# Performance work log

Hardware: AMD Instinct MI355X
Metric: run time of the kernel (lower is better)

The kernel has to match this reference:

```python
import jax, jax.numpy as jnp
import numpy as np

H = 16          # attention_head_num
DH = 64         # attention_head_size
D = H * DH      # out_dim / model dim
SIZE_PER_HEAD = 64  # scaling denominator (init arg, used as sqrt divisor)


def setup_inputs() -> dict:
    key = jax.random.key(0)
    ks = jax.random.split(key, 12)
    B, S = 2, 2048
    scale = 1.0 / np.sqrt(D)
    inp = {
        "qx": jax.random.normal(ks[0], (B, S, D), dtype=jnp.float32),
        "kx": jax.random.normal(ks[1], (B, S, D), dtype=jnp.float32),
        "vx": jax.random.normal(ks[2], (B, S, D), dtype=jnp.float32),
        "Wq": jax.random.normal(ks[3], (D, D), dtype=jnp.float32) * scale,
        "bq": jnp.zeros((D,), dtype=jnp.float32),
        "Wk": jax.random.normal(ks[4], (D, D), dtype=jnp.float32) * scale,
        "bk": jnp.zeros((D,), dtype=jnp.float32),
        "Wv": jax.random.normal(ks[5], (D, D), dtype=jnp.float32) * scale,
        "bv": jnp.zeros((D,), dtype=jnp.float32),
        "Wo": jax.random.normal(ks[6], (D, D), dtype=jnp.float32) * scale,
        "bo": jnp.zeros((D,), dtype=jnp.float32),
    }
    return inp


def reference(qx, kx, vx, Wq, bq, Wk, bk, Wv, bv, Wo, bo):
    B, Sq, _ = qx.shape
    Sk = kx.shape[1]
    # QKV projections
    q = qx @ Wq + bq  # [B,Sq,D]
    k = kx @ Wk + bk  # [B,Sk,D]
    v = vx @ Wv + bv  # [B,Sk,D]
    # split heads -> [B,H,S,DH]
    q = q.reshape(B, Sq, H, DH).transpose(0, 2, 1, 3)
    k = k.reshape(B, Sk, H, DH).transpose(0, 2, 1, 3)
    v = v.reshape(B, Sk, H, DH).transpose(0, 2, 1, 3)
    # scores [B,H,Sq,Sk]; NOTE: original divides by sqrt(size_per_head)
    scores = jnp.einsum("bhqd,bhkd->bhqk", q, k) / jnp.sqrt(
        jnp.asarray(SIZE_PER_HEAD, dtype=q.dtype)
    )
    probs = jax.nn.softmax(scores, axis=-1)
    ctx = jnp.einsum("bhqk,bhkd->bhqd", probs, v)  # [B,H,Sq,DH]
    ctx = ctx.transpose(0, 2, 1, 3).reshape(B, Sq, D)
    return ctx @ Wo + bo
```

## Files before the change

kernel.cpp:

```cpp
#include <hip/hip_runtime.h>

typedef _Float16 half_t;
typedef _Float16 half8 __attribute__((ext_vector_type(8)));
typedef __fp16 fp16x2 __attribute__((ext_vector_type(2)));
typedef float f32x16 __attribute__((ext_vector_type(16)));
typedef float f32x4v __attribute__((ext_vector_type(4)));
typedef unsigned uint2v __attribute__((ext_vector_type(2)));

#define MFMA32(A, B, C) __builtin_amdgcn_mfma_f32_32x32x16_f16(A, B, C, 0, 0, 0)

#if __has_builtin(__builtin_amdgcn_exp2f)
#define EXP2F(x) __builtin_amdgcn_exp2f(x)
#else
#define EXP2F(x) exp2f(x)
#endif

static constexpr int S = 2048;
static constexpr int D = 1024;
static constexpr float QSCALE = 0.18033688011112042f;


__device__ __forceinline__ void gload_lds16(const void* g, void* l) {
    __builtin_amdgcn_global_load_lds(
        (const __attribute__((address_space(1))) unsigned int*)g,
        (__attribute__((address_space(3))) unsigned int*)l, 16, 0, 0);
}

__global__ __launch_bounds__(256) void cvtw(
    const float* __restrict__ x0, const float* __restrict__ x1, const float* __restrict__ x2,
    const float* __restrict__ w0, const float* __restrict__ w1,
    const float* __restrict__ w2, const float* __restrict__ w3,
    half_t* __restrict__ o0, half_t* __restrict__ o1, half_t* __restrict__ o2,
    half_t* __restrict__ wt)
{
    __shared__ char sm[33280];
    int y = blockIdx.y;
    int t = threadIdx.x;
    if (y < 3) {
        float (*tile)[65] = (float(*)[65])sm;
        const float* src = (y == 0) ? x0 : (y == 1) ? x1 : x2;
        half_t* dst = (y == 0) ? o0 : (y == 1) ? o1 : o2;
        int mt = blockIdx.x >> 4, kt = blockIdx.x & 15;
        const float* sbase = src + (size_t)(mt * 128) * D + kt * 64;
        int rr = t >> 4, col = (t & 15) * 4;
#pragma unroll
        for (int p = 0; p < 8; ++p) {
            int row = rr + p * 16;
            f32x4v v = *(const f32x4v*)(sbase + (size_t)row * D + col);
            tile[row][col] = v[0]; tile[row][col + 1] = v[1];
            tile[row][col + 2] = v[2]; tile[row][col + 3] = v[3];
        }
        __syncthreads();
        int c = t >> 5, r0 = t & 31;
        half_t* dbase = dst + ((size_t)(mt * 16 + kt)) * 8192;
#pragma unroll
        for (int i = 0; i < 4; ++i) {
            int row = r0 + 32 * i;
            half8 h;
#pragma unroll
            for (int j = 0; j < 8; ++j) h[j] = (half_t)tile[row][c * 8 + j];
            *(half8*)(dbase + ((size_t)c * 128 + row) * 8) = h;
        }
    } else {
        float (*tile)[129] = (float(*)[129])sm;
        int w = blockIdx.x >> 7;
        const float* W = (w == 0) ? w0 : (w == 1) ? w1 : (w == 2) ? w2 : w3;
        int idx = blockIdx.x & 127;
        int nt = idx >> 4, kt = idx & 15;
        const float* sbase = W + (size_t)(kt * 64) * D + nt * 128;
        int kr = t >> 5, col = (t & 31) * 4;
#pragma unroll
        for (int p = 0; p < 8; ++p) {
            int k = kr + p * 8;
            f32x4v v = *(const f32x4v*)(sbase + (size_t)k * D + col);
            tile[k][col] = v[0]; tile[k][col + 1] = v[1];
            tile[k][col + 2] = v[2]; tile[k][col + 3] = v[3];
        }
        __syncthreads();
        int c = t >> 5, r0 = t & 31;
        half_t* dbase = wt + (size_t)w * 1048576 + ((size_t)(nt * 16 + kt)) * 8192;
#pragma unroll
        for (int i = 0; i < 4; ++i) {
            int n = r0 + 32 * i;
            half8 h;
#pragma unroll
            for (int j = 0; j < 8; ++j) h[j] = (half_t)tile[c * 8 + j][n];
            *(half8*)(dbase + ((size_t)c * 128 + n) * 8) = h;
        }
    }
}

__global__ __launch_bounds__(256, 4) void gemm_qkv(
    const half_t* __restrict__ a0, const half_t* __restrict__ a1, const half_t* __restrict__ a2,
    const half_t* __restrict__ wt,
    const float* __restrict__ b0, const float* __restrict__ b1, const float* __restrict__ b2,
    half_t* __restrict__ qh, half_t* __restrict__ kh, half_t* __restrict__ vt)
{
    __shared__ char smem[32768];
    half_t* As = (half_t*)smem;
    half_t* Bs = (half_t*)(smem + 16384);
    int z = blockIdx.z;
    const half_t* A = (z == 0) ? a0 : (z == 1) ? a1 : a2;
    const half_t* BT = wt + (size_t)z * 1048576;
    const float* bias = (z == 0) ? b0 : (z == 1) ? b1 : b2;
    int L = blockIdx.x;
    int w = L >> 3;
    int mt = (L & 7) * 4 + (w & 3);
    int nt8 = w >> 2;
    int m0 = mt * 128, n0 = nt8 * 128;
    int tid = threadIdx.x, lane = tid & 63, wave = tid >> 6;
    int ml = lane & 31, hi = lane >> 5;
    int wm = (wave & 1) * 64, wn = (wave >> 1) * 64;

    f32x16 acc00 = {}, acc01 = {}, acc10 = {}, acc11 = {};

    for (int kt = 0; kt < 16; ++kt) {
        __syncthreads();
        const half_t* Aslab = A + ((size_t)(mt * 16 + kt)) * 8192;
        const half_t* Bslab = BT + ((size_t)(nt8 * 16 + kt)) * 8192;
#pragma unroll
        for (int j = 0; j < 4; ++j) {
            int s = wave * 4 + j;
            gload_lds16(Aslab + s * 512 + lane * 8, As + s * 512);
            gload_lds16(Bslab + s * 512 + lane * 8, Bs + s * 512);
        }
        __syncthreads();
#pragma unroll
        for (int ks = 0; ks < 4; ++ks) {
            int co = (2 * ks + hi) * 128;
            half8 af0 = *(const half8*)(As + (size_t)(co + wm + ml) * 8);
            half8 af1 = *(const half8*)(As + (size_t)(co + wm + 32 + ml) * 8);
            half8 bf0 = *(const half8*)(Bs + (size_t)(co + wn + ml) * 8);
            half8 bf1 = *(const half8*)(Bs + (size_t)(co + wn + 32 + ml) * 8);
            acc00 = MFMA32(af0, bf0, acc00);
            acc01 = MFMA32(af0, bf1, acc01);
            acc10 = MFMA32(af1, bf0, acc10);
            acc11 = MFMA32(af1, bf1, acc11);
        }
    }

    __syncthreads();
    half_t* buf = (half_t*)smem;
#pragma unroll
    for (int nt = 0; nt < 2; ++nt) {
        int nl = wn + nt * 32 + ml;
        float bv = bias[n0 + nl];
        int hh = nl >> 6, c = (nl >> 3) & 7, j = nl & 7, dd = nl & 63;
#pragma unroll
        for (int mt2 = 0; mt2 < 2; ++mt2) {
            f32x16 av = (mt2 == 0) ? (nt == 0 ? acc00 : acc01) : (nt == 0 ? acc10 : acc11);
#pragma unroll
            for (int r = 0; r < 16; ++r) {
                int rl = wm + mt2 * 32 + 4 * hi + (r & 3) + 8 * (r >> 2);
                float v = av[r] + bv;
                if (z == 0) v *= QSCALE;
                if (z <= 1) {
                    buf[((rl * 2 + hh) * 8 + (c ^ (rl & 7))) * 8 + j] = (half_t)v;
                } else {
                    int cc = rl >> 3, js = rl & 7;
                    buf[((dd * 2 + hh) * 16 + (cc ^ (dd & 7))) * 8 + js] = (half_t)v;
                }
            }
        }
    }
    __syncthreads();
    int bq_ = m0 >> 11, skt = (m0 >> 7) & 15, h0 = n0 >> 6;
    half_t* dstm = (z == 0) ? qh : (z == 1) ? kh : vt;
#pragma unroll
    for (int i = 0; i < 8; ++i) {
        int o = tid + 256 * i;
        int hh = o >> 10;
        half_t* gdst = dstm + ((size_t)(bq_ * 16 + h0 + hh)) * 131072 + (size_t)skt * 8192;
        half8 v8;
        int off;
        if (z <= 1) {
            int c = (o >> 7) & 7, r = o & 127;
            v8 = *(const half8*)(buf + (((r * 2 + hh) * 8 + (c ^ (r & 7))) * 8));
            off = (c * 128 + r) * 8;
        } else {
            int cc = (o >> 6) & 15, dd = o & 63;
            v8 = *(const half8*)(buf + (((dd * 2 + hh) * 16 + (cc ^ (dd & 7))) * 8));
            off = (cc * 64 + dd) * 8;
        }
        *(half8*)(gdst + off) = v8;
    }
}

__global__ __launch_bounds__(256, 4) void gemm_out(
    const half_t* __restrict__ A, const half_t* __restrict__ BT,
    const float* __restrict__ bias, float* __restrict__ out)
{
    __shared__ char smem[32768];
    half_t* As = (half_t*)smem;
    half_t* Bs = (half_t*)(smem + 16384);
    int L = blockIdx.x;
    int w = L >> 3;
    int mt = (L & 7) * 4 + (w & 3);
    int nt8 = w >> 2;
    int m0 = mt * 128, n0 = nt8 * 128;
    int tid = threadIdx.x, lane = tid & 63, wave = tid >> 6;
    int ml = lane & 31, hi = lane >> 5;
    int wm = (wave & 1) * 64, wn = (wave >> 1) * 64;

    f32x16 acc00 = {}, acc01 = {}, acc10 = {}, acc11 = {};

    for (int kt = 0; kt < 16; ++kt) {
        __syncthreads();
        const half_t* Aslab = A + ((size_t)(mt * 16 + kt)) * 8192;
        const half_t* Bslab = BT + ((size_t)(nt8 * 16 + kt)) * 8192;
#pragma unroll
        for (int j = 0; j < 4; ++j) {
            int s = wave * 4 + j;
            gload_lds16(Aslab + s * 512 + lane * 8, As + s * 512);
            gload_lds16(Bslab + s * 512 + lane * 8, Bs + s * 512);
        }
        __syncthreads();
#pragma unroll
        for (int ks = 0; ks < 4; ++ks) {
            int co = (2 * ks + hi) * 128;
            half8 af0 = *(const half8*)(As + (size_t)(co + wm + ml) * 8);
            half8 af1 = *(const half8*)(As + (size_t)(co + wm + 32 + ml) * 8);
            half8 bf0 = *(const half8*)(Bs + (size_t)(co + wn + ml) * 8);
            half8 bf1 = *(const half8*)(Bs + (size_t)(co + wn + 32 + ml) * 8);
            acc00 = MFMA32(af0, bf0, acc00);
            acc01 = MFMA32(af0, bf1, acc01);
            acc10 = MFMA32(af1, bf0, acc10);
            acc11 = MFMA32(af1, bf1, acc11);
        }
    }

#pragma unroll
    for (int nt = 0; nt < 2; ++nt) {
        int n = n0 + wn + nt * 32 + ml;
        float bv = bias[n];
#pragma unroll
        for (int mt2 = 0; mt2 < 2; ++mt2) {
            f32x16 av = (mt2 == 0) ? (nt == 0 ? acc00 : acc01) : (nt == 0 ? acc10 : acc11);
            int rbase = m0 + wm + mt2 * 32 + 4 * hi;
#pragma unroll
            for (int r = 0; r < 16; ++r) {
                int row = rbase + (r & 3) + 8 * (r >> 2);
                out[(size_t)row * D + n] = av[r] + bv;
            }
        }
    }
}

__global__ __launch_bounds__(512, 4) void attn(
    const half_t* __restrict__ qh, const half_t* __restrict__ kh,
    const half_t* __restrict__ vt, half_t* __restrict__ ctx)
{
    __shared__ char smem[65536];

    int L = blockIdx.x;
    int slot = L >> 3;
    int bh = (L & 7) + 8 * (slot >> 4);
    int sq = slot & 15;
    int b_ = bh >> 4, h = bh & 15;

    int tid = threadIdx.x, lane = tid & 63, wave = tid >> 6;
    int ml = lane & 31, hi = lane >> 5;
    int qq = wave & 3, th = wave >> 2;
    const half_t* qslab = qh + (size_t)bh * 131072 + (size_t)sq * 8192;
    const half_t* khead = kh + (size_t)bh * 131072;
    const half_t* vhead = vt + (size_t)bh * 131072;

    {
        half_t* QB = (half_t*)(smem + 32768);
        half_t* K0 = (half_t*)(smem);
        half_t* V0 = (half_t*)(smem + 16384);
#pragma unroll
        for (int j = 0; j < 2; ++j) {
            int s = wave * 2 + j;
            gload_lds16(qslab + s * 512 + lane * 8, QB + s * 512);
            gload_lds16(khead + s * 512 + lane * 8, K0 + s * 512);
            gload_lds16(vhead + s * 512 + lane * 8, V0 + s * 512);
        }
    }
    __syncthreads();
    half8 qf[4];
    {
        half_t* QB = (half_t*)(smem + 32768);
#pragma unroll
        for (int ks = 0; ks < 4; ++ks)
            qf[ks] = *(const half8*)(QB + ((size_t)((2 * ks + hi) * 128 + qq * 32 + ml)) * 8);
    }
    __syncthreads();

    f32x16 oacc[2] = {};
    float lsumA = 0.0f, lsumB = 0.0f;
    fp16x2 one2; one2.x = (__fp16)1.0f; one2.y = (__fp16)1.0f;
    const f32x16 sinit = {-10.0f, -10.0f, -10.0f, -10.0f, -10.0f, -10.0f, -10.0f, -10.0f,
                          -10.0f, -10.0f, -10.0f, -10.0f, -10.0f, -10.0f, -10.0f, -10.0f};

    int t0 = th * 2, t1 = th * 2 + 1;

    for (int it = 0; it < 16; ++it) {
        int bb = it & 1;
        if (it < 15) {
            const half_t* kslab = khead + (size_t)(it + 1) * 8192;
            const half_t* vslab = vhead + (size_t)(it + 1) * 8192;
            half_t* Kd = (half_t*)(smem + (bb ^ 1) * 32768);
            half_t* Vd = (half_t*)(smem + 16384 + (bb ^ 1) * 32768);
#pragma unroll
            for (int j = 0; j < 2; ++j) {
                int s = wave * 2 + j;
                gload_lds16(kslab + s * 512 + lane * 8, Kd + s * 512);
                gload_lds16(vslab + s * 512 + lane * 8, Vd + s * 512);
            }
        }
        half_t* Ks  = (half_t*)(smem + bb * 32768);
        half_t* VTs = (half_t*)(smem + 16384 + bb * 32768);

        f32x16 sv0 = sinit, sv1 = sinit;
        __builtin_amdgcn_s_setprio(1);
#pragma unroll
        for (int ks = 0; ks < 4; ++ks) {
            half8 kf0 = *(const half8*)(Ks + ((size_t)((2 * ks + hi) * 128 + t0 * 32 + ml)) * 8);
            half8 kf1 = *(const half8*)(Ks + ((size_t)((2 * ks + hi) * 128 + t1 * 32 + ml)) * 8);
            sv0 = MFMA32(kf0, qf[ks], sv0);
            sv1 = MFMA32(kf1, qf[ks], sv1);
        }
        __builtin_amdgcn_s_setprio(0);

        unsigned pkv0[8];
        {
            float lsA = lsumA;
#pragma unroll
            for (int j = 0; j < 8; ++j) {
                float pa = EXP2F(sv0[2 * j]);
                float pb = EXP2F(sv0[2 * j + 1]);
#if __has_builtin(__builtin_amdgcn_cvt_pkrtz)
                fp16x2 h2 = __builtin_amdgcn_cvt_pkrtz(pa, pb);
#else
                fp16x2 h2; h2.x = (__fp16)pa; h2.y = (__fp16)pb;
#endif
                pkv0[j] = __builtin_bit_cast(unsigned, h2);
#if __has_builtin(__builtin_amdgcn_fdot2)
                lsA = __builtin_amdgcn_fdot2(h2, one2, lsA, false);
#else
                lsA += pa + pb;
#endif
            }
            lsumA = lsA;
        }

#pragma unroll
        for (int kp = 0; kp < 2; ++kp) {
            union { unsigned u[4]; half8 h; } fr;
#if __has_builtin(__builtin_amdgcn_permlane32_swap)
            uint2v w0 = __builtin_amdgcn_permlane32_swap(pkv0[4 * kp + 0], pkv0[4 * kp + 2], false, false);
            uint2v w1 = __builtin_amdgcn_permlane32_swap(pkv0[4 * kp + 1], pkv0[4 * kp + 3], false, false);
            fr.u[0] = w0.x; fr.u[1] = w1.x; fr.u[2] = w0.y; fr.u[3] = w1.y;
#else
            unsigned e0 = pkv0[4 * kp + 0], e1 = pkv0[4 * kp + 1];
            unsigned o0 = pkv0[4 * kp + 2], o1 = pkv0[4 * kp + 3];
            unsigned s0u = hi ? e0 : o0, s1u = hi ? e1 : o1;
            unsigned k0u = hi ? o0 : e0, k1u = hi ? o1 : e1;
            unsigned r0 = __shfl_xor(s0u, 32, 64);
            unsigned r1 = __shfl_xor(s1u, 32, 64);
            fr.u[0] = hi ? r0 : k0u; fr.u[1] = hi ? r1 : k1u;
            fr.u[2] = hi ? k0u : r0; fr.u[3] = hi ? k1u : r1;
#endif
            __builtin_amdgcn_s_setprio(1);
#pragma unroll
            for (int dt = 0; dt < 2; ++dt) {
                half8 vf = *(const half8*)(VTs + ((size_t)((4 * t0 + 2 * kp + hi) * 64 + dt * 32 + ml)) * 8);
                oacc[dt] = MFMA32(fr.h, vf, oacc[dt]);
            }
            __builtin_amdgcn_s_setprio(0);
        }

        unsigned pkv1[8];
        {
            float lsB = lsumB;
#pragma unroll
            for (int j = 0; j < 8; ++j) {
                float pa = EXP2F(sv1[2 * j]);
                float pb = EXP2F(sv1[2 * j + 1]);
#if __has_builtin(__builtin_amdgcn_cvt_pkrtz)
                fp16x2 h2 = __builtin_amdgcn_cvt_pkrtz(pa, pb);
#else
                fp16x2 h2; h2.x = (__fp16)pa; h2.y = (__fp16)pb;
#endif
                pkv1[j] = __builtin_bit_cast(unsigned, h2);
#if __has_builtin(__builtin_amdgcn_fdot2)
                lsB = __builtin_amdgcn_fdot2(h2, one2, lsB, false);
#else
                lsB += pa + pb;
#endif
            }
            lsumB = lsB;
        }

#pragma unroll
        for (int kp = 0; kp < 2; ++kp) {
            union { unsigned u[4]; half8 h; } fr;
#if __has_builtin(__builtin_amdgcn_permlane32_swap)
            uint2v w0 = __builtin_amdgcn_permlane32_swap(pkv1[4 * kp + 0], pkv1[4 * kp + 2], false, false);
            uint2v w1 = __builtin_amdgcn_permlane32_swap(pkv1[4 * kp + 1], pkv1[4 * kp + 3], false, false);
            fr.u[0] = w0.x; fr.u[1] = w1.x; fr.u[2] = w0.y; fr.u[3] = w1.y;
#else
            unsigned e0 = pkv1[4 * kp + 0], e1 = pkv1[4 * kp + 1];
            unsigned o0 = pkv1[4 * kp + 2], o1 = pkv1[4 * kp + 3];
            unsigned s0u = hi ? e0 : o0, s1u = hi ? e1 : o1;
            unsigned k0u = hi ? o0 : e0, k1u = hi ? o1 : e1;
            unsigned r0 = __shfl_xor(s0u, 32, 64);
            unsigned r1 = __shfl_xor(s1u, 32, 64);
            fr.u[0] = hi ? r0 : k0u; fr.u[1] = hi ? r1 : k1u;
            fr.u[2] = hi ? k0u : r0; fr.u[3] = hi ? k1u : r1;
#endif
            __builtin_amdgcn_s_setprio(1);
#pragma unroll
            for (int dt = 0; dt < 2; ++dt) {
                half8 vf = *(const half8*)(VTs + ((size_t)((4 * t1 + 2 * kp + hi) * 64 + dt * 32 + ml)) * 8);
                oacc[dt] = MFMA32(fr.h, vf, oacc[dt]);
            }
            __builtin_amdgcn_s_setprio(0);
        }

        __syncthreads();
    }

    float lsum = lsumA + lsumB;
    float lt = lsum + __shfl_xor(lsum, 32, 64);

    float* OB = (float*)(smem + (size_t)qq * 8192);
    if (th == 1) {
#pragma unroll
        for (int dt = 0; dt < 2; ++dt)
#pragma unroll
            for (int r = 0; r < 16; ++r) {
                int q = 4 * hi + (r & 3) + 8 * (r >> 2);
                OB[q * 64 + dt * 32 + ml] = oacc[dt][r];
            }
    }
    __syncthreads();
    if (th == 0) {
#pragma unroll
        for (int dt = 0; dt < 2; ++dt)
#pragma unroll
            for (int r = 0; r < 16; ++r) {
                int q = 4 * hi + (r & 3) + 8 * (r >> 2);
                oacc[dt][r] += OB[q * 64 + dt * 32 + ml];
            }
    }
    __syncthreads();
    float* Lbuf = (float*)(smem + 32768);
    if (th == 1 && hi == 0) Lbuf[qq * 32 + ml] = lt;
    __syncthreads();
    if (th == 0 && hi == 0) Lbuf[qq * 32 + ml] += lt;
    __syncthreads();
    if (th == 0) {
        half_t* cslab = ctx + ((size_t)((b_ * 16 + sq) * 16 + h)) * 8192;
#pragma unroll
        for (int dt = 0; dt < 2; ++dt)
#pragma unroll
            for (int r = 0; r < 16; ++r) {
                int qw = 4 * hi + (r & 3) + 8 * (r >> 2);
                int q = qq * 32 + qw;
                int d = dt * 32 + ml;
                float linv = __builtin_amdgcn_rcpf(Lbuf[q]);
                cslab[((d >> 3) * 128 + q) * 8 + (d & 7)] =
                    (half_t)(oacc[dt][r] * linv);
            }
    }
}

extern "C" void kernel_launch(void* const* d_in, const int* in_sizes, int n_in,
                              void* d_out, int out_size, void* d_ws, size_t ws_size,
                              hipStream_t stream)
{
    const float* qx = (const float*)d_in[0];
    const float* kx = (const float*)d_in[1];
    const float* vx = (const float*)d_in[2];
    const float* Wq = (const float*)d_in[3];
    const float* bq = (const float*)d_in[4];
    const float* Wk = (const float*)d_in[5];
    const float* bk = (const float*)d_in[6];
    const float* Wv = (const float*)d_in[7];
    const float* bv = (const float*)d_in[8];
    const float* Wo = (const float*)d_in[9];
    const float* bo = (const float*)d_in[10];
    float* out = (float*)d_out;

    half_t* ws = (half_t*)d_ws;
    const size_t NT = (size_t)4096 * 1024;
    half_t* qxh = ws;
    half_t* kxh = qxh + NT;
    half_t* vxh = kxh + NT;
    half_t* wt = vxh + NT;
    half_t* qh = wt + (size_t)4 * 1048576;
    half_t* kh = qh + NT;
    half_t* vtr = kh + NT;
    half_t* ctx = vtr + NT;

    cvtw<<<dim3(512, 4), 256, 0, stream>>>(qx, kx, vx, Wq, Wk, Wv, Wo, qxh, kxh, vxh, wt);
    gemm_qkv<<<dim3(256, 1, 3), 256, 0, stream>>>(qxh, kxh, vxh, wt, bq, bk, bv, qh, kh, vtr);
    attn<<<dim3(512, 1, 1), 512, 0, stream>>>(qh, kh, vtr, ctx);
    gemm_out<<<dim3(256, 1, 1), 256, 0, stream>>>(ctx, wt + (size_t)3 * 1048576, bo, out);
}
```

Before: 215.2 us.

## Fuse all four stages into one persistent kernel with grid barriers

Measured after the change: 610.7 us. +183.8%, slower.

```diff
diff --git a/kernel.cpp b/kernel.cpp
--- a/kernel.cpp
+++ b/kernel.cpp
@@ -26,89 +26,43 @@
         (__attribute__((address_space(3))) unsigned int*)l, 16, 0, 0);
 }
 
-__global__ __launch_bounds__(256) void cvtw(
-    const float* __restrict__ x0, const float* __restrict__ x1, const float* __restrict__ x2,
-    const float* __restrict__ w0, const float* __restrict__ w1,
-    const float* __restrict__ w2, const float* __restrict__ w3,
-    half_t* __restrict__ o0, half_t* __restrict__ o1, half_t* __restrict__ o2,
-    half_t* __restrict__ wt)
-{
-    __shared__ char sm[33280];
-    int y = blockIdx.y;
-    int t = threadIdx.x;
-    if (y < 3) {
-        float (*tile)[65] = (float(*)[65])sm;
-        const float* src = (y == 0) ? x0 : (y == 1) ? x1 : x2;
-        half_t* dst = (y == 0) ? o0 : (y == 1) ? o1 : o2;
-        int mt = blockIdx.x >> 4, kt = blockIdx.x & 15;
-        const float* sbase = src + (size_t)(mt * 128) * D + kt * 64;
-        int rr = t >> 4, col = (t & 15) * 4;
-#pragma unroll
-        for (int p = 0; p < 8; ++p) {
-            int row = rr + p * 16;
-            f32x4v v = *(const f32x4v*)(sbase + (size_t)row * D + col);
-            tile[row][col] = v[0]; tile[row][col + 1] = v[1];
-            tile[row][col + 2] = v[2]; tile[row][col + 3] = v[3];
-        }
-        __syncthreads();
-        int c = t >> 5, r0 = t & 31;
-        half_t* dbase = dst + ((size_t)(mt * 16 + kt)) * 8192;
-#pragma unroll
-        for (int i = 0; i < 4; ++i) {
-            int row = r0 + 32 * i;
-            half8 h;
-#pragma unroll
-            for (int j = 0; j < 8; ++j) h[j] = (half_t)tile[row][c * 8 + j];
-            *(half8*)(dbase + ((size_t)c * 128 + row) * 8) = h;
-        }
-    } else {
-        float (*tile)[129] = (float(*)[129])sm;
-        int w = blockIdx.x >> 7;
-        const float* W = (w == 0) ? w0 : (w == 1) ? w1 : (w == 2) ? w2 : w3;
-        int idx = blockIdx.x & 127;
-        int nt = idx >> 4, kt = idx & 15;
-        const float* sbase = W + (size_t)(kt * 64) * D + nt * 128;
-        int kr = t >> 5, col = (t & 31) * 4;
-#pragma unroll
-        for (int p = 0; p < 8; ++p) {
-            int k = kr + p * 8;
-            f32x4v v = *(const f32x4v*)(sbase + (size_t)k * D + col);
-            tile[k][col] = v[0]; tile[k][col + 1] = v[1];
-            tile[k][col + 2] = v[2]; tile[k][col + 3] = v[3];
-        }
-        __syncthreads();
-        int c = t >> 5, r0 = t & 31;
-        half_t* dbase = wt + (size_t)w * 1048576 + ((size_t)(nt * 16 + kt)) * 8192;
-#pragma unroll
-        for (int i = 0; i < 4; ++i) {
-            int n = r0 + 32 * i;
-            half8 h;
-#pragma unroll
-            for (int j = 0; j < 8; ++j) h[j] = (half_t)tile[c * 8 + j][n];
-            *(half8*)(dbase + ((size_t)c * 128 + n) * 8) = h;
-        }
-    }
+__device__ __forceinline__ void gridbar(unsigned* bar, int idx) {
+    __syncthreads();
+    if (threadIdx.x == 0) {
+        __threadfence();
+        unsigned* cnt  = bar + idx * 16;
+        unsigned* flag = bar + idx * 16 + 8;
+        unsigned old = atomicAdd(cnt, 1u);
+        if (old == 511u) {
+            __hip_atomic_store(flag, 1u, __ATOMIC_RELEASE, __HIP_MEMORY_SCOPE_AGENT);
+        } else {
+            while (__hip_atomic_load(flag, __ATOMIC_ACQUIRE, __HIP_MEMORY_SCOPE_AGENT) == 0u)
+                __builtin_amdgcn_s_sleep(2);
+        }
+    }
+    __syncthreads();
+    __threadfence();
 }
 
-__global__ __launch_bounds__(256, 4) void gemm_qkv(
+__device__ __forceinline__ void gemm_tile_qkv(
+    int job, int t, char* sm, bool active,
     const half_t* __restrict__ a0, const half_t* __restrict__ a1, const half_t* __restrict__ a2,
     const half_t* __restrict__ wt,
     const float* __restrict__ b0, const float* __restrict__ b1, const float* __restrict__ b2,
-    half_t* __restrict__ qh, half_t* __restrict__ kh, half_t* __restrict__ vt)
+    half_t* __restrict__ qh, half_t* __restrict__ kh, half_t* __restrict__ vtb)
 {
-    __shared__ char smem[32768];
-    half_t* As = (half_t*)smem;
-    half_t* Bs = (half_t*)(smem + 16384);
-    int z = blockIdx.z;
+    half_t* As = (half_t*)sm;
+    half_t* Bs = (half_t*)(sm + 16384);
+    int z = job >> 8;
+    int L = job & 255;
     const half_t* A = (z == 0) ? a0 : (z == 1) ? a1 : a2;
     const half_t* BT = wt + (size_t)z * 1048576;
     const float* bias = (z == 0) ? b0 : (z == 1) ? b1 : b2;
-    int L = blockIdx.x;
     int w = L >> 3;
     int mt = (L & 7) * 4 + (w & 3);
     int nt8 = w >> 2;
     int m0 = mt * 128, n0 = nt8 * 128;
-    int tid = threadIdx.x, lane = tid & 63, wave = tid >> 6;
+    int lane = t & 63, wave = t >> 6;
     int ml = lane & 31, hi = lane >> 5;
     int wm = (wave & 1) * 64, wn = (wave >> 1) * 64;
 
@@ -116,89 +70,96 @@
 
     for (int kt = 0; kt < 16; ++kt) {
         __syncthreads();
-        const half_t* Aslab = A + ((size_t)(mt * 16 + kt)) * 8192;
-        const half_t* Bslab = BT + ((size_t)(nt8 * 16 + kt)) * 8192;
-#pragma unroll
-        for (int j = 0; j < 4; ++j) {
-            int s = wave * 4 + j;
-            gload_lds16(Aslab + s * 512 + lane * 8, As + s * 512);
-            gload_lds16(Bslab + s * 512 + lane * 8, Bs + s * 512);
-        }
-        __syncthreads();
-#pragma unroll
-        for (int ks = 0; ks < 4; ++ks) {
-            int co = (2 * ks + hi) * 128;
-            half8 af0 = *(const half8*)(As + (size_t)(co + wm + ml) * 8);
-            half8 af1 = *(const half8*)(As + (size_t)(co + wm + 32 + ml) * 8);
-            half8 bf0 = *(const half8*)(Bs + (size_t)(co + wn + ml) * 8);
-            half8 bf1 = *(const half8*)(Bs + (size_t)(co + wn + 32 + ml) * 8);
-            acc00 = MFMA32(af0, bf0, acc00);
-            acc01 = MFMA32(af0, bf1, acc01);
-            acc10 = MFMA32(af1, bf0, acc10);
-            acc11 = MFMA32(af1, bf1, acc11);
+        if (active) {
+            const half_t* Aslab = A + ((size_t)(mt * 16 + kt)) * 8192;
+            const half_t* Bslab = BT + ((size_t)(nt8 * 16 + kt)) * 8192;
+#pragma unroll
+            for (int j = 0; j < 4; ++j) {
+                int s = wave * 4 + j;
+                gload_lds16(Aslab + s * 512 + lane * 8, As + s * 512);
+                gload_lds16(Bslab + s * 512 + lane * 8, Bs + s * 512);
+            }
+        }
+        __syncthreads();
+        if (active) {
+#pragma unroll
+            for (int ks = 0; ks < 4; ++ks) {
+                int co = (2 * ks + hi) * 128;
+                half8 af0 = *(const half8*)(As + (size_t)(co + wm + ml) * 8);
+                half8 af1 = *(const half8*)(As + (size_t)(co + wm + 32 + ml) * 8);
+                half8 bf0 = *(const half8*)(Bs + (size_t)(co + wn + ml) * 8);
+                half8 bf1 = *(const half8*)(Bs + (size_t)(co + wn + 32 + ml) * 8);
+                acc00 = MFMA32(af0, bf0, acc00);
+                acc01 = MFMA32(af0, bf1, acc01);
+                acc10 = MFMA32(af1, bf0, acc10);
+                acc11 = MFMA32(af1, bf1, acc11);
+            }
         }
     }
 
     __syncthreads();
-    half_t* buf = (half_t*)smem;
-#pragma unroll
-    for (int nt = 0; nt < 2; ++nt) {
-        int nl = wn + nt * 32 + ml;
-        float bv = bias[n0 + nl];
-        int hh = nl >> 6, c = (nl >> 3) & 7, j = nl & 7, dd = nl & 63;
-#pragma unroll
-        for (int mt2 = 0; mt2 < 2; ++mt2) {
-            f32x16 av = (mt2 == 0) ? (nt == 0 ? acc00 : acc01) : (nt == 0 ? acc10 : acc11);
-#pragma unroll
-            for (int r = 0; r < 16; ++r) {
-                int rl = wm + mt2 * 32 + 4 * hi + (r & 3) + 8 * (r >> 2);
-                float v = av[r] + bv;
-                if (z == 0) v *= QSCALE;
-                if (z <= 1) {
-                    buf[((rl * 2 + hh) * 8 + (c ^ (rl & 7))) * 8 + j] = (half_t)v;
-                } else {
-                    int cc = rl >> 3, js = rl & 7;
-                    buf[((dd * 2 + hh) * 16 + (cc ^ (dd & 7))) * 8 + js] = (half_t)v;
+    half_t* buf = (half_t*)sm;
+    if (active) {
+#pragma unroll
+        for (int nt = 0; nt < 2; ++nt) {
+            int nl = wn + nt * 32 + ml;
+            float bv = bias[n0 + nl];
+            int hh = nl >> 6, c = (nl >> 3) & 7, j = nl & 7, dd = nl & 63;
+#pragma unroll
+            for (int mt2 = 0; mt2 < 2; ++mt2) {
+                f32x16 av = (mt2 == 0) ? (nt == 0 ? acc00 : acc01) : (nt == 0 ? acc10 : acc11);
+#pragma unroll
+                for (int r = 0; r < 16; ++r) {
+                    int rl = wm + mt2 * 32 + 4 * hi + (r & 3) + 8 * (r >> 2);
+                    float v = av[r] + bv;
+                    if (z == 0) v *= QSCALE;
+                    if (z <= 1) {
+                        buf[((rl * 2 + hh) * 8 + (c ^ (rl & 7))) * 8 + j] = (half_t)v;
+                    } else {
+                        int cc = rl >> 3, js = rl & 7;
+                        buf[((dd * 2 + hh) * 16 + (cc ^ (dd & 7))) * 8 + js] = (half_t)v;
+                    }
                 }
             }
         }
     }
     __syncthreads();
-    int bq_ = m0 >> 11, skt = (m0 >> 7) & 15, h0 = n0 >> 6;
-    half_t* dstm = (z == 0) ? qh : (z == 1) ? kh : vt;
-#pragma unroll
-    for (int i = 0; i < 8; ++i) {
-        int o = tid + 256 * i;
-        int hh = o >> 10;
-        half_t* gdst = dstm + ((size_t)(bq_ * 16 + h0 + hh)) * 131072 + (size_t)skt * 8192;
-        half8 v8;
-        int off;
-        if (z <= 1) {
-            int c = (o >> 7) & 7, r = o & 127;
-            v8 = *(const half8*)(buf + (((r * 2 + hh) * 8 + (c ^ (r & 7))) * 8));
-            off = (c * 128 + r) * 8;
-        } else {
-            int cc = (o >> 6) & 15, dd = o & 63;
-            v8 = *(const half8*)(buf + (((dd * 2 + hh) * 16 + (cc ^ (dd & 7))) * 8));
-            off = (cc * 64 + dd) * 8;
-        }
-        *(half8*)(gdst + off) = v8;
+    if (active) {
+        int bq_ = m0 >> 11, skt = (m0 >> 7) & 15, h0 = n0 >> 6;
+        half_t* dstm = (z == 0) ? qh : (z == 1) ? kh : vtb;
+#pragma unroll
+        for (int i = 0; i < 8; ++i) {
+            int o = t + 256 * i;
+            int hh = o >> 10;
+            half_t* gdst = dstm + ((size_t)(bq_ * 16 + h0 + hh)) * 131072 + (size_t)skt * 8192;
+            half8 v8;
+            int off;
+            if (z <= 1) {
+                int c = (o >> 7) & 7, r = o & 127;
+                v8 = *(const half8*)(buf + (((r * 2 + hh) * 8 + (c ^ (r & 7))) * 8));
+                off = (c * 128 + r) * 8;
+            } else {
+                int cc = (o >> 6) & 15, dd = o & 63;
+                v8 = *(const half8*)(buf + (((dd * 2 + hh) * 16 + (cc ^ (dd & 7))) * 8));
+                off = (cc * 64 + dd) * 8;
+            }
+            *(half8*)(gdst + off) = v8;
+        }
     }
 }
 
-__global__ __launch_bounds__(256, 4) void gemm_out(
+__device__ __forceinline__ void gemm_tile_out(
+    int L, int t, char* sm, bool active,
     const half_t* __restrict__ A, const half_t* __restrict__ BT,
     const float* __restrict__ bias, float* __restrict__ out)
 {
-    __shared__ char smem[32768];
-    half_t* As = (half_t*)smem;
-    half_t* Bs = (half_t*)(smem + 16384);
-    int L = blockIdx.x;
+    half_t* As = (half_t*)sm;
+    half_t* Bs = (half_t*)(sm + 16384);
     int w = L >> 3;
     int mt = (L & 7) * 4 + (w & 3);
     int nt8 = w >> 2;
     int m0 = mt * 128, n0 = nt8 * 128;
-    int tid = threadIdx.x, lane = tid & 63, wave = tid >> 6;
+    int lane = t & 63, wave = t >> 6;
     int ml = lane & 31, hi = lane >> 5;
     int wm = (wave & 1) * 64, wn = (wave >> 1) * 64;
 
@@ -206,264 +167,356 @@
 
     for (int kt = 0; kt < 16; ++kt) {
         __syncthreads();
-        const half_t* Aslab = A + ((size_t)(mt * 16 + kt)) * 8192;
-        const half_t* Bslab = BT + ((size_t)(nt8 * 16 + kt)) * 8192;
-#pragma unroll
-        for (int j = 0; j < 4; ++j) {
-            int s = wave * 4 + j;
-            gload_lds16(Aslab + s * 512 + lane * 8, As + s * 512);
-            gload_lds16(Bslab + s * 512 + lane * 8, Bs + s * 512);
-        }
-        __syncthreads();
-#pragma unroll
-        for (int ks = 0; ks < 4; ++ks) {
-            int co = (2 * ks + hi) * 128;
-            half8 af0 = *(const half8*)(As + (size_t)(co + wm + ml) * 8);
-            half8 af1 = *(const half8*)(As + (size_t)(co + wm + 32 + ml) * 8);
-            half8 bf0 = *(const half8*)(Bs + (size_t)(co + wn + ml) * 8);
-            half8 bf1 = *(const half8*)(Bs + (size_t)(co + wn + 32 + ml) * 8);
-            acc00 = MFMA32(af0, bf0, acc00);
-            acc01 = MFMA32(af0, bf1, acc01);
-            acc10 = MFMA32(af1, bf0, acc10);
-            acc11 = MFMA32(af1, bf1, acc11);
-        }
-    }
-
-#pragma unroll
-    for (int nt = 0; nt < 2; ++nt) {
-        int n = n0 + wn + nt * 32 + ml;
-        float bv = bias[n];
-#pragma unroll
-        for (int mt2 = 0; mt2 < 2; ++mt2) {
-            f32x16 av = (mt2 == 0) ? (nt == 0 ? acc00 : acc01) : (nt == 0 ? acc10 : acc11);
-            int rbase = m0 + wm + mt2 * 32 + 4 * hi;
-#pragma unroll
-            for (int r = 0; r < 16; ++r) {
-                int row = rbase + (r & 3) + 8 * (r >> 2);
-                out[(size_t)row * D + n] = av[r] + bv;
+        if (active) {
+            const half_t* Aslab = A + ((size_t)(mt * 16 + kt)) * 8192;
+            const half_t* Bslab = BT + ((size_t)(nt8 * 16 + kt)) * 8192;
+#pragma unroll
+            for (int j = 0; j < 4; ++j) {
+                int s = wave * 4 + j;
+                gload_lds16(Aslab + s * 512 + lane * 8, As + s * 512);
+                gload_lds16(Bslab + s * 512 + lane * 8, Bs + s * 512);
+            }
+        }
+        __syncthreads();
+        if (active) {
+#pragma unroll
+            for (int ks = 0; ks < 4; ++ks) {
+                int co = (2 * ks + hi) * 128;
+                half8 af0 = *(const half8*)(As + (size_t)(co + wm + ml) * 8);
+                half8 af1 = *(const half8*)(As + (size_t)(co + wm + 32 + ml) * 8);
+                half8 bf0 = *(const half8*)(Bs + (size_t)(co + wn + ml) * 8);
+                half8 bf1 = *(const half8*)(Bs + (size_t)(co + wn + 32 + ml) * 8);
+                acc00 = MFMA32(af0, bf0, acc00);
+                acc01 = MFMA32(af0, bf1, acc01);
+                acc10 = MFMA32(af1, bf0, acc10);
+                acc11 = MFMA32(af1, bf1, acc11);
+            }
+        }
+    }
+
+    if (active) {
+#pragma unroll
+        for (int nt = 0; nt < 2; ++nt) {
+            int n = n0 + wn + nt * 32 + ml;
+            float bv = bias[n];
+#pragma unroll
+            for (int mt2 = 0; mt2 < 2; ++mt2) {
+                f32x16 av = (mt2 == 0) ? (nt == 0 ? acc00 : acc01) : (nt == 0 ? acc10 : acc11);
+                int rbase = m0 + wm + mt2 * 32 + 4 * hi;
+#pragma unroll
+                for (int r = 0; r < 16; ++r) {
+                    int row = rbase + (r & 3) + 8 * (r >> 2);
+                    out[(size_t)row * D + n] = av[r] + bv;
+                }
             }
         }
     }
 }
 
-__global__ __launch_bounds__(512, 4) void attn(
-    const half_t* __restrict__ qh, const half_t* __restrict__ kh,
-    const half_t* __restrict__ vt, half_t* __restrict__ ctx)
+__global__ __launch_bounds__(512, 4) void fused(
+    const float* __restrict__ qx, const float* __restrict__ kx, const float* __restrict__ vx,
+    const float* __restrict__ Wq, const float* __restrict__ bq,
+    const float* __restrict__ Wk, const float* __restrict__ bk,
+    const float* __restrict__ Wv, const float* __restrict__ bv,
+    const float* __restrict__ Wo, const float* __restrict__ bo,
+    float* __restrict__ out,
+    half_t* __restrict__ qxh, half_t* __restrict__ kxh, half_t* __restrict__ vxh,
+    half_t* __restrict__ wt, half_t* __restrict__ qh, half_t* __restrict__ kh,
+    half_t* __restrict__ vtr, half_t* __restrict__ ctx, unsigned* __restrict__ bar)
 {
     __shared__ char smem[65536];
-
-    int L = blockIdx.x;
-    int slot = L >> 3;
-    int bh = (L & 7) + 8 * (slot >> 4);
-    int sq = slot & 15;
-    int b_ = bh >> 4, h = bh & 15;
-
-    int tid = threadIdx.x, lane = tid & 63, wave = tid >> 6;
-    int ml = lane & 31, hi = lane >> 5;
-    int qq = wave & 3, th = wave >> 2;
-    const half_t* qslab = qh + (size_t)bh * 131072 + (size_t)sq * 8192;
-    const half_t* khead = kh + (size_t)bh * 131072;
-    const half_t* vhead = vt + (size_t)bh * 131072;
+    int bid = blockIdx.x;
+    int t = threadIdx.x;
+    int sb = t >> 8, t256 = t & 255;
+
+    for (int job = bid; job < 2048; job += 512) {
+        __syncthreads();
+        int y = job >> 9, x = job & 511;
+        if (y < 3) {
+            float (*tile)[65] = (float(*)[65])smem;
+            const float* src = (y == 0) ? qx : (y == 1) ? kx : vx;
+            half_t* dst = (y == 0) ? qxh : (y == 1) ? kxh : vxh;
+            int mt = x >> 4, kt = x & 15;
+            const float* sbase = src + (size_t)(mt * 128) * D + kt * 64;
+            int rr = t >> 4, col = (t & 15) * 4;
+#pragma unroll
+            for (int p = 0; p < 4; ++p) {
+                int row = rr + p * 32;
+                f32x4v v = *(const f32x4v*)(sbase + (size_t)row * D + col);
+                tile[row][col] = v[0]; tile[row][col + 1] = v[1];
+                tile[row][col + 2] = v[2]; tile[row][col + 3] = v[3];
+            }
+            __syncthreads();
+            int c = t >> 6, r0 = t & 63;
+            half_t* dbase = dst + ((size_t)(mt * 16 + kt)) * 8192;
+#pragma unroll
+            for (int i = 0; i < 2; ++i) {
+                int row = r0 + 64 * i;
+                half8 h;
+#pragma unroll
+                for (int j = 0; j < 8; ++j) h[j] = (half_t)tile[row][c * 8 + j];
+                *(half8*)(dbase + ((size_t)c * 128 + row) * 8) = h;
+            }
+        } else {
+            float (*tile)[129] = (float(*)[129])smem;
+            int w = x >> 7;
+            const float* W = (w == 0) ? Wq : (w == 1) ? Wk : (w == 2) ? Wv : Wo;
+            int idx = x & 127;
+            int nt = idx >> 4, kt = idx & 15;
+            const float* sbase = W + (size_t)(kt * 64) * D + nt * 128;
+            int kr = t >> 5, col = (t & 31) * 4;
+#pragma unroll
+            for (int p = 0; p < 4; ++p) {
+                int k = kr + p * 16;
+                f32x4v v = *(const f32x4v*)(sbase + (size_t)k * D + col);
+                tile[k][col] = v[0]; tile[k][col + 1] = v[1];
+                tile[k][col + 2] = v[2]; tile[k][col + 3] = v[3];
+            }
+            __syncthreads();
+            int c = t >> 6, r0 = t & 63;
+            half_t* dbase = wt + (size_t)w * 1048576 + ((size_t)(nt * 16 + kt)) * 8192;
+#pragma unroll
+            for (int i = 0; i < 2; ++i) {
+                int n = r0 + 64 * i;
+                half8 h;
+#pragma unroll
+                for (int j = 0; j < 8; ++j) h[j] = (half_t)tile[c * 8 + j][n];
+                *(half8*)(dbase + ((size_t)c * 128 + n) * 8) = h;
+            }
+        }
+    }
+    gridbar(bar, 0);
 
     {
-        half_t* QB = (half_t*)(smem + 32768);
-        half_t* K0 = (half_t*)(smem);
-        half_t* V0 = (half_t*)(smem + 16384);
-#pragma unroll
-        for (int j = 0; j < 2; ++j) {
-            int s = wave * 2 + j;
-            gload_lds16(qslab + s * 512 + lane * 8, QB + s * 512);
-            gload_lds16(khead + s * 512 + lane * 8, K0 + s * 512);
-            gload_lds16(vhead + s * 512 + lane * 8, V0 + s * 512);
-        }
-    }
-    __syncthreads();
-    half8 qf[4];
+        int job; bool active;
+        if (sb == 0) { job = bid; active = true; }
+        else { job = 512 + (bid >> 1); active = ((bid & 1) == 0); }
+        gemm_tile_qkv(active ? job : 0, t256, smem + (size_t)sb * 32768, active,
+                      qxh, kxh, vxh, wt, bq, bk, bv, qh, kh, vtr);
+    }
+    gridbar(bar, 1);
+
     {
-        half_t* QB = (half_t*)(smem + 32768);
-#pragma unroll
-        for (int ks = 0; ks < 4; ++ks)
-            qf[ks] = *(const half8*)(QB + ((size_t)((2 * ks + hi) * 128 + qq * 32 + ml)) * 8);
-    }
-    __syncthreads();
-
-    f32x16 oacc[2] = {};
-    float lsumA = 0.0f, lsumB = 0.0f;
-    fp16x2 one2; one2.x = (__fp16)1.0f; one2.y = (__fp16)1.0f;
-    const f32x16 sinit = {-10.0f, -10.0f, -10.0f, -10.0f, -10.0f, -10.0f, -10.0f, -10.0f,
-                          -10.0f, -10.0f, -10.0f, -10.0f, -10.0f, -10.0f, -10.0f, -10.0f};
-
-    int t0 = th * 2, t1 = th * 2 + 1;
-
-    for (int it = 0; it < 16; ++it) {
-        int bb = it & 1;
-        if (it < 15) {
-            const half_t* kslab = khead + (size_t)(it + 1) * 8192;
-            const half_t* vslab = vhead + (size_t)(it + 1) * 8192;
-            half_t* Kd = (half_t*)(smem + (bb ^ 1) * 32768);
-            half_t* Vd = (half_t*)(smem + 16384 + (bb ^ 1) * 32768);
+        int L = bid;
+        int slot = L >> 3;
+        int bh = (L & 7) + 8 * (slot >> 4);
+        int sq = slot & 15;
+        int b_ = bh >> 4, h = bh & 15;
+
+        int lane = t & 63, wave = t >> 6;
+        int ml = lane & 31, hi = lane >> 5;
+        int qq = wave & 3, th = wave >> 2;
+        const half_t* qslab = qh + (size_t)bh * 131072 + (size_t)sq * 8192;
+        const half_t* khead = kh + (size_t)bh * 131072;
+        const half_t* vhead = vtr + (size_t)bh * 131072;
+
+        {
+            half_t* QB = (half_t*)(smem + 32768);
+            half_t* K0 = (half_t*)(smem);
+            half_t* V0 = (half_t*)(smem + 16384);
 #pragma unroll
             for (int j = 0; j < 2; ++j) {
                 int s = wave * 2 + j;
-                gload_lds16(kslab + s * 512 + lane * 8, Kd + s * 512);
-                gload_lds16(vslab + s * 512 + lane * 8, Vd + s * 512);
-            }
-        }
-        half_t* Ks  = (half_t*)(smem + bb * 32768);
-        half_t* VTs = (half_t*)(smem + 16384 + bb * 32768);
-
-        f32x16 sv0 = sinit, sv1 = sinit;
-        __builtin_amdgcn_s_setprio(1);
-#pragma unroll
-        for (int ks = 0; ks < 4; ++ks) {
-            half8 kf0 = *(const half8*)(Ks + ((size_t)((2 * ks + hi) * 128 + t0 * 32 + ml)) * 8);
-            half8 kf1 = *(const half8*)(Ks + ((size_t)((2 * ks + hi) * 128 + t1 * 32 + ml)) * 8);
-            sv0 = MFMA32(kf0, qf[ks], sv0);
-            sv1 = MFMA32(kf1, qf[ks], sv1);
-        }
-        __builtin_amdgcn_s_setprio(0);
-
-        unsigned pkv0[8];
+                gload_lds16(qslab + s * 512 + lane * 8, QB + s * 512);
+                gload_lds16(khead + s * 512 + lane * 8, K0 + s * 512);
+                gload_lds16(vhead + s * 512 + lane * 8, V0 + s * 512);
+            }
+        }
+        __syncthreads();
+        half8 qf[4];
         {
-            float lsA = lsumA;
-#pragma unroll
-            for (int j = 0; j < 8; ++j) {
-                float pa = EXP2F(sv0[2 * j]);
-                float pb = EXP2F(sv0[2 * j + 1]);
+            half_t* QB = (half_t*)(smem + 32768);
+#pragma unroll
+            for (int ks = 0; ks < 4; ++ks)
+                qf[ks] = *(const half8*)(QB + ((size_t)((2 * ks + hi) * 128 + qq * 32 + ml)) * 8);
+        }
+        __syncthreads();
+
+        f32x16 oacc[2] = {};
+        float lsumA = 0.0f, lsumB = 0.0f;
+        fp16x2 one2; one2.x = (__fp16)1.0f; one2.y = (__fp16)1.0f;
+        const f32x16 sinit = {-10.0f, -10.0f, -10.0f, -10.0f, -10.0f, -10.0f, -10.0f, -10.0f,
+                              -10.0f, -10.0f, -10.0f, -10.0f, -10.0f, -10.0f, -10.0f, -10.0f};
+
+        int t0 = th * 2, t1 = th * 2 + 1;
+
+        for (int it = 0; it < 16; ++it) {
+            int bb = it & 1;
+            if (it < 15) {
+                const half_t* kslab = khead + (size_t)(it + 1) * 8192;
+                const half_t* vslab = vhead + (size_t)(it + 1) * 8192;
+                half_t* Kd = (half_t*)(smem + (bb ^ 1) * 32768);
+                half_t* Vd = (half_t*)(smem + 16384 + (bb ^ 1) * 32768);
+#pragma unroll
+                for (int j = 0; j < 2; ++j) {
+                    int s = wave * 2 + j;
+                    gload_lds16(kslab + s * 512 + lane * 8, Kd + s * 512);
+                    gload_lds16(vslab + s * 512 + lane * 8, Vd + s * 512);
+                }
+            }
+            half_t* Ks  = (half_t*)(smem + bb * 32768);
+            half_t* VTs = (half_t*)(smem + 16384 + bb * 32768);
+
+            f32x16 sv0 = sinit, sv1 = sinit;
+            __builtin_amdgcn_s_setprio(1);
+#pragma unroll
+            for (int ks = 0; ks < 4; ++ks) {
+                half8 kf0 = *(const half8*)(Ks + ((size_t)((2 * ks + hi) * 128 + t0 * 32 + ml)) * 8);
+                half8 kf1 = *(const half8*)(Ks + ((size_t)((2 * ks + hi) * 128 + t1 * 32 + ml)) * 8);
+                sv0 = MFMA32(kf0, qf[ks], sv0);
+                sv1 = MFMA32(kf1, qf[ks], sv1);
+            }
+            __builtin_amdgcn_s_setprio(0);
+
+            unsigned pkv0[8];
+            {
+                float lsA = lsumA;
+#pragma unroll
+                for (int j = 0; j < 8; ++j) {
+                    float pa = EXP2F(sv0[2 * j]);
+                    float pb = EXP2F(sv0[2 * j + 1]);
 #if __has_builtin(__builtin_amdgcn_cvt_pkrtz)
-                fp16x2 h2 = __builtin_amdgcn_cvt_pkrtz(pa, pb);
-#else
-                fp16x2 h2; h2.x = (__fp16)pa; h2.y = (__fp16)pb;
-#endif
-                pkv0[j] = __builtin_bit_cast(unsigned, h2);
+                    fp16x2 h2 = __builtin_amdgcn_cvt_pkrtz(pa, pb);
+#else
+                    fp16x2 h2; h2.x = (__fp16)pa; h2.y = (__fp16)pb;
+#endif
+                    pkv0[j] = __builtin_bit_cast(unsigned, h2);
 #if __has_builtin(__builtin_amdgcn_fdot2)
-                lsA = __builtin_amdgcn_fdot2(h2, one2, lsA, false);
-#else
-                lsA += pa + pb;
-#endif
-            }
-            lsumA = lsA;
-        }
-
-#pragma unroll
-        for (int kp = 0; kp < 2; ++kp) {
-            union { unsigned u[4]; half8 h; } fr;
+                    lsA = __builtin_amdgcn_fdot2(h2, one2, lsA, false);
+#else
+                    lsA += pa + pb;
+#endif
+                }
+                lsumA = lsA;
+            }
+
+#pragma unroll
+            for (int kp = 0; kp < 2; ++kp) {
+                union { unsigned u[4]; half8 h; } fr;
 #if __has_builtin(__builtin_amdgcn_permlane32_swap)
-            uint2v w0 = __builtin_amdgcn_permlane32_swap(pkv0[4 * kp + 0], pkv0[4 * kp + 2], false, false);
-            uint2v w1 = __builtin_amdgcn_permlane32_swap(pkv0[4 * kp + 1], pkv0[4 * kp + 3], false, false);
-            fr.u[0] = w0.x; fr.u[1] = w1.x; fr.u[2] = w0.y; fr.u[3] = w1.y;
-#else
-            unsigned e0 = pkv0[4 * kp + 0], e1 = pkv0[4 * kp + 1];
-            unsigned o0 = pkv0[4 * kp + 2], o1 = pkv0[4 * kp + 3];
-            unsigned s0u = hi ? e0 : o0, s1u = hi ? e1 : o1;
-            unsigned k0u = hi ? o0 : e0, k1u = hi ? o1 : e1;
-            unsigned r0 = __shfl_xor(s0u, 32, 64);
-            unsigned r1 = __shfl_xor(s1u, 32, 64);
-            fr.u[0] = hi ? r0 : k0u; fr.u[1] = hi ? r1 : k1u;
-            fr.u[2] = hi ? k0u : r0; fr.u[3] = hi ? k1u : r1;
-#endif
-            __builtin_amdgcn_s_setprio(1);
-#pragma unroll
-            for (int dt = 0; dt < 2; ++dt) {
-                half8 vf = *(const half8*)(VTs + ((size_t)((4 * t0 + 2 * kp + hi) * 64 + dt * 32 + ml)) * 8);
-                oacc[dt] = MFMA32(fr.h, vf, oacc[dt]);
-            }
-            __builtin_amdgcn_s_setprio(0);
-        }
-
-        unsigned pkv1[8];
-        {
-            float lsB = lsumB;
-#pragma unroll
-            for (int j = 0; j < 8; ++j) {
-                float pa = EXP2F(sv1[2 * j]);
-                float pb = EXP2F(sv1[2 * j + 1]);
+                uint2v w0 = __builtin_amdgcn_permlane32_swap(pkv0[4 * kp + 0], pkv0[4 * kp + 2], false, false);
+                uint2v w1 = __builtin_amdgcn_permlane32_swap(pkv0[4 * kp + 1], pkv0[4 * kp + 3], false, false);
+                fr.u[0] = w0.x; fr.u[1] = w1.x; fr.u[2] = w0.y; fr.u[3] = w1.y;
+#else
+                unsigned e0 = pkv0[4 * kp + 0], e1 = pkv0[4 * kp + 1];
+                unsigned o0 = pkv0[4 * kp + 2], o1 = pkv0[4 * kp + 3];
+                unsigned s0u = hi ? e0 : o0, s1u = hi ? e1 : o1;
+                unsigned k0u = hi ? o0 : e0, k1u = hi ? o1 : e1;
+                unsigned r0 = __shfl_xor(s0u, 32, 64);
+                unsigned r1 = __shfl_xor(s1u, 32, 64);
+                fr.u[0] = hi ? r0 : k0u; fr.u[1] = hi ? r1 : k1u;
+                fr.u[2] = hi ? k0u : r0; fr.u[3] = hi ? k1u : r1;
+#endif
+                __builtin_amdgcn_s_setprio(1);
+#pragma unroll
+                for (int dt = 0; dt < 2; ++dt) {
+                    half8 vf = *(const half8*)(VTs + ((size_t)((4 * t0 + 2 * kp + hi) * 64 + dt * 32 + ml)) * 8);
+                    oacc[dt] = MFMA32(fr.h, vf, oacc[dt]);
+                }
+                __builtin_amdgcn_s_setprio(0);
+            }
+
+            unsigned pkv1[8];
+            {
+                float lsB = lsumB;
+#pragma unroll
+                for (int j = 0; j < 8; ++j) {
+                    float pa = EXP2F(sv1[2 * j]);
+                    float pb = EXP2F(sv1[2 * j + 1]);
 #if __has_builtin(__builtin_amdgcn_cvt_pkrtz)
-                fp16x2 h2 = __builtin_amdgcn_cvt_pkrtz(pa, pb);
-#else
-                fp16x2 h2; h2.x = (__fp16)pa; h2.y = (__fp16)pb;
-#endif
-                pkv1[j] = __builtin_bit_cast(unsigned, h2);
+                    fp16x2 h2 = __builtin_amdgcn_cvt_pkrtz(pa, pb);
+#else
+                    fp16x2 h2; h2.x = (__fp16)pa; h2.y = (__fp16)pb;
+#endif
+                    pkv1[j] = __builtin_bit_cast(unsigned, h2);
 #if __has_builtin(__builtin_amdgcn_fdot2)
-                lsB = __builtin_amdgcn_fdot2(h2, one2, lsB, false);
-#else
-                lsB += pa + pb;
-#endif
-            }
-            lsumB = lsB;
-        }
-
-#pragma unroll
-        for (int kp = 0; kp < 2; ++kp) {
-            union { unsigned u[4]; half8 h; } fr;
+                    lsB = __builtin_amdgcn_fdot2(h2, one2, lsB, false);
+#else
+                    lsB += pa + pb;
+#endif
+                }
+                lsumB = lsB;
+            }
+
+#pragma unroll
+            for (int kp = 0; kp < 2; ++kp) {
+                union { unsigned u[4]; half8 h; } fr;
 #if __has_builtin(__builtin_amdgcn_permlane32_swap)
-            uint2v w0 = __builtin_amdgcn_permlane32_swap(pkv1[4 * kp + 0], pkv1[4 * kp + 2], false, false);
-            uint2v w1 = __builtin_amdgcn_permlane32_swap(pkv1[4 * kp + 1], pkv1[4 * kp + 3], false, false);
-            fr.u[0] = w0.x; fr.u[1] = w1.x; fr.u[2] = w0.y; fr.u[3] = w1.y;
-#else
-            unsigned e0 = pkv1[4 * kp + 0], e1 = pkv1[4 * kp + 1];
-            unsigned o0 = pkv1[4 * kp + 2], o1 = pkv1[4 * kp + 3];
-            unsigned s0u = hi ? e0 : o0, s1u = hi ? e1 : o1;
-            unsigned k0u = hi ? o0 : e0, k1u = hi ? o1 : e1;
-            unsigned r0 = __shfl_xor(s0u, 32, 64);
-            unsigned r1 = __shfl_xor(s1u, 32, 64);
-            fr.u[0] = hi ? r0 : k0u; fr.u[1] = hi ? r1 : k1u;
-            fr.u[2] = hi ? k0u : r0; fr.u[3] = hi ? k1u : r1;
-#endif
-            __builtin_amdgcn_s_setprio(1);
-#pragma unroll
-            for (int dt = 0; dt < 2; ++dt) {
-                half8 vf = *(const half8*)(VTs + ((size_t)((4 * t1 + 2 * kp + hi) * 64 + dt * 32 + ml)) * 8);
-                oacc[dt] = MFMA32(fr.h, vf, oacc[dt]);
-            }
-            __builtin_amdgcn_s_setprio(0);
-        }
-
-        __syncthreads();
-    }
-
-    float lsum = lsumA + lsumB;
-    float lt = lsum + __shfl_xor(lsum, 32, 64);
-
-    float* OB = (float*)(smem + (size_t)qq * 8192);
-    if (th == 1) {
-#pragma unroll
-        for (int dt = 0; dt < 2; ++dt)
-#pragma unroll
-            for (int r = 0; r < 16; ++r) {
-                int q = 4 * hi + (r & 3) + 8 * (r >> 2);
-                OB[q * 64 + dt * 32 + ml] = oacc[dt][r];
-            }
-    }
-    __syncthreads();
-    if (th == 0) {
-#pragma unroll
-        for (int dt = 0; dt < 2; ++dt)
-#pragma unroll
-            for (int r = 0; r < 16; ++r) {
-                int q = 4 * hi + (r & 3) + 8 * (r >> 2);
-                oacc[dt][r] += OB[q * 64 + dt * 32 + ml];
-            }
-    }
-    __syncthreads();
-    float* Lbuf = (float*)(smem + 32768);
-    if (th == 1 && hi == 0) Lbuf[qq * 32 + ml] = lt;
-    __syncthreads();
-    if (th == 0 && hi == 0) Lbuf[qq * 32 + ml] += lt;
-    __syncthreads();
-    if (th == 0) {
-        half_t* cslab = ctx + ((size_t)((b_ * 16 + sq) * 16 + h)) * 8192;
-#pragma unroll
-        for (int dt = 0; dt < 2; ++dt)
-#pragma unroll
-            for (int r = 0; r < 16; ++r) {
-                int qw = 4 * hi + (r & 3) + 8 * (r >> 2);
-                int q = qq * 32 + qw;
-                int d = dt * 32 + ml;
-                float linv = __builtin_amdgcn_rcpf(Lbuf[q]);
-                cslab[((d >> 3) * 128 + q) * 8 + (d & 7)] =
-                    (half_t)(oacc[dt][r] * linv);
-            }
+                uint2v w0 = __builtin_amdgcn_permlane32_swap(pkv1[4 * kp + 0], pkv1[4 * kp + 2], false, false);
+                uint2v w1 = __builtin_amdgcn_permlane32_swap(pkv1[4 * kp + 1], pkv1[4 * kp + 3], false, false);
+                fr.u[0] = w0.x; fr.u[1] = w1.x; fr.u[2] = w0.y; fr.u[3] = w1.y;
+#else
+                unsigned e0 = pkv1[4 * kp + 0], e1 = pkv1[4 * kp + 1];
+                unsigned o0 = pkv1[4 * kp + 2], o1 = pkv1[4 * kp + 3];
+                unsigned s0u = hi ? e0 : o0, s1u = hi ? e1 : o1;
+                unsigned k0u = hi ? o0 : e0, k1u = hi ? o1 : e1;
+                unsigned r0 = __shfl_xor(s0u, 32, 64);
+                unsigned r1 = __shfl_xor(s1u, 32, 64);
+                fr.u[0] = hi ? r0 : k0u; fr.u[1] = hi ? r1 : k1u;
+                fr.u[2] = hi ? k0u : r0; fr.u[3] = hi ? k1u : r1;
+#endif
+                __builtin_amdgcn_s_setprio(1);
+#pragma unroll
+                for (int dt = 0; dt < 2; ++dt) {
+                    half8 vf = *(const half8*)(VTs + ((size_t)((4 * t1 + 2 * kp + hi) * 64 + dt * 32 + ml)) * 8);
+                    oacc[dt] = MFMA32(fr.h, vf, oacc[dt]);
+                }
+                __builtin_amdgcn_s_setprio(0);
+            }
+
+            __syncthreads();
+        }
+
+        float lsum = lsumA + lsumB;
+        float lt = lsum + __shfl_xor(lsum, 32, 64);
+
+        float* OB = (float*)(smem + (size_t)qq * 8192);
+        if (th == 1) {
+#pragma unroll
+            for (int dt = 0; dt < 2; ++dt)
+#pragma unroll
+                for (int r = 0; r < 16; ++r) {
+                    int q = 4 * hi + (r & 3) + 8 * (r >> 2);
+                    OB[q * 64 + dt * 32 + ml] = oacc[dt][r];
+                }
+        }
+        __syncthreads();
+        if (th == 0) {
+#pragma unroll
+            for (int dt = 0; dt < 2; ++dt)
+#pragma unroll
+                for (int r = 0; r < 16; ++r) {
+                    int q = 4 * hi + (r & 3) + 8 * (r >> 2);
+                    oacc[dt][r] += OB[q * 64 + dt * 32 + ml];
+                }
+        }
+        __syncthreads();
+        float* Lbuf = (float*)(smem + 32768);
+        if (th == 1 && hi == 0) Lbuf[qq * 32 + ml] = lt;
+        __syncthreads();
+        if (th == 0 && hi == 0) Lbuf[qq * 32 + ml] += lt;
+        __syncthreads();
+        if (th == 0) {
+            half_t* cslab = ctx + ((size_t)((b_ * 16 + sq) * 16 + h)) * 8192;
+#pragma unroll
+            for (int dt = 0; dt < 2; ++dt)
+#pragma unroll
+                for (int r = 0; r < 16; ++r) {
+                    int qw = 4 * hi + (r & 3) + 8 * (r >> 2);
+                    int q = qq * 32 + qw;
+                    int d = dt * 32 + ml;
+                    float linv = __builtin_amdgcn_rcpf(Lbuf[q]);
+                    cslab[((d >> 3) * 128 + q) * 8 + (d & 7)] =
+                        (half_t)(oacc[dt][r] * linv);
+                }
+        }
+    }
+    gridbar(bar, 2);
+
+    {
+        bool active = (sb == 0) && ((bid & 1) == 0);
+        gemm_tile_out(bid >> 1, t256, smem + (size_t)sb * 32768, active,
+                      ctx, wt + (size_t)3 * 1048576, bo, out);
     }
 }
 
@@ -494,9 +547,10 @@
     half_t* kh = qh + NT;
     half_t* vtr = kh + NT;
     half_t* ctx = vtr + NT;
-
-    cvtw<<<dim3(512, 4), 256, 0, stream>>>(qx, kx, vx, Wq, Wk, Wv, Wo, qxh, kxh, vxh, wt);
-    gemm_qkv<<<dim3(256, 1, 3), 256, 0, stream>>>(qxh, kxh, vxh, wt, bq, bk, bv, qh, kh, vtr);
-    attn<<<dim3(512, 1, 1), 512, 0, stream>>>(qh, kh, vtr, ctx);
-    gemm_out<<<dim3(256, 1, 1), 256, 0, stream>>>(ctx, wt + (size_t)3 * 1048576, bo, out);
+    unsigned* bar = (unsigned*)(ctx + NT);
+
+    hipMemsetAsync((void*)bar, 0, 256, stream);
+    fused<<<dim3(512), dim3(512), 0, stream>>>(
+        qx, kx, vx, Wq, bq, Wk, bk, Wv, bv, Wo, bo, out,
+        qxh, kxh, vxh, wt, qh, kh, vtr, ctx, bar);
 }
```
